# Kernel tuning notes

Hardware: AMD Instinct MI355X
Metric: run time of the kernel (lower is better)

## Reference

```python
import jax, jax.numpy as jnp
import numpy as np

N_NODES = 100000
N_EDGES = 640000
F_IN = 128
HID = 128
N_CLS = 40


def _glorot(key, fan_in, fan_out):
    lim = float(np.sqrt(6.0 / (fan_in + fan_out)))
    return jax.random.uniform(key, (fan_in, fan_out), jnp.float32, -lim, lim)


def setup_inputs() -> dict:
    key = jax.random.key(0)
    ks = jax.random.split(key, 10)
    x = jax.random.normal(ks[0], (N_NODES, F_IN), jnp.float32)
    edge_index = jax.random.randint(ks[1], (2, N_EDGES), 0, N_NODES, jnp.int64 if jax.config.jax_enable_x64 else jnp.int32)
    W1 = _glorot(ks[2], F_IN, HID)
    W2 = _glorot(ks[3], HID, HID)
    W3 = _glorot(ks[4], HID, HID)
    W4 = _glorot(ks[5], HID, N_CLS)
    b1 = jnp.zeros((HID,), jnp.float32)
    b2 = jnp.zeros((HID,), jnp.float32)
    b3 = jnp.zeros((HID,), jnp.float32)
    b4 = jnp.zeros((N_CLS,), jnp.float32)
    return {"x": x, "edge_index": edge_index,
            "W1": W1, "b1": b1, "W2": W2, "b2": b2,
            "W3": W3, "b3": b3, "W4": W4, "b4": b4}


def _prep_edges(edge_index, n):
    # add self-loops, compute symmetric normalization deg^{-1/2}[src]*deg^{-1/2}[dst]
    loop = jnp.arange(n, dtype=edge_index.dtype)
    src = jnp.concatenate([edge_index[0], loop])
    dst = jnp.concatenate([edge_index[1], loop])
    deg = jax.ops.segment_sum(jnp.ones_like(dst, jnp.float32), dst, num_segments=n)
    dinv = jnp.where(deg > 0, jax.lax.rsqrt(deg), 0.0)
    norm = dinv[src] * dinv[dst]  # [E + n]
    return src, dst, norm


def _gcn_conv(x, W, b, src, dst, norm, n):
    h = x @ W                      # dense linear transform [n, out]
    msg = h[src] * norm[:, None]   # gather + scale over edges
    out = jax.ops.segment_sum(msg, dst, num_segments=n)  # scatter-add
    return out + b


def reference(x, edge_index, W1, b1, W2, b2, W3, b3, W4, b4):
    n = x.shape[0]
    src, dst, norm = _prep_edges(edge_index, n)
    h = jax.nn.relu(_gcn_conv(x, W1, b1, src, dst, norm, n))
    h = jax.nn.relu(_gcn_conv(h, W2, b2, src, dst, norm, n))
    h = jax.nn.relu(_gcn_conv(h, W3, b3, src, dst, norm, n))
    h = _gcn_conv(h, W4, b4, src, dst, norm, n)
    return jax.nn.log_softmax(h, axis=1)
```

## Files before the change

### kernel.cpp

```cpp
#include <hip/hip_runtime.h>
#include <math.h>

#define N_NODES 100000
#define N_EDGES 640000

typedef __bf16 bf16x8 __attribute__((ext_vector_type(8)));
typedef float f32x4 __attribute__((ext_vector_type(4)));

__device__ __forceinline__ unsigned short f2b(float x) {
  unsigned int u = __float_as_uint(x);
  u = (u + 0x7FFFu + ((u >> 16) & 1u)) >> 16;
  return (unsigned short)u;
}
__device__ __forceinline__ float blo(unsigned int v) { return __uint_as_float(v << 16); }
__device__ __forceinline__ float bhi(unsigned int v) { return __uint_as_float(v & 0xFFFF0000u); }


__global__ __launch_bounds__(256) void k_count(const int* __restrict__ dst, int* __restrict__ deg, int e) {
  int i = blockIdx.x * 256 + threadIdx.x;
  if (i < e) atomicAdd(&deg[dst[i]], 1);
}

__global__ __launch_bounds__(256) void k_alloc(const int* __restrict__ deg, int* __restrict__ row_ptr,
                                               int* __restrict__ fillpos, int* __restrict__ col,
                                               float* __restrict__ dinv, int* __restrict__ counter, int n) {
  __shared__ int sdata[256];
  __shared__ int sbase;
  int tid = threadIdx.x;
  int i = blockIdx.x * 256 + tid;
  int d = (i < n) ? deg[i] : 0;
  sdata[tid] = d;
  __syncthreads();
  for (int off = 1; off < 256; off <<= 1) {
    int v = (tid >= off) ? sdata[tid - off] : 0;
    __syncthreads();
    sdata[tid] += v;
    __syncthreads();
  }
  if (tid == 255) sbase = atomicAdd(counter, sdata[255]);
  __syncthreads();
  int base = sbase;
  if (i < n) {
    int rp = base + sdata[tid] - d;
    row_ptr[i] = rp;
    fillpos[i] = rp + 1;
    col[rp] = i;
    dinv[i] = rsqrtf((float)d);
  }
}

__global__ __launch_bounds__(256) void k_fill(const int* __restrict__ src, const int* __restrict__ dst,
                                              int* __restrict__ fillpos, int* __restrict__ col, int e) {
  int i = blockIdx.x * 256 + threadIdx.x;
  if (i < e) {
    int d = dst[i];
    int p = atomicAdd(&fillpos[d], 1);
    col[p] = src[i];
  }
}


__global__ __launch_bounds__(256) void k_prep0(const float* __restrict__ W1, const float* __restrict__ W2,
                                               const float* __restrict__ W3, const float* __restrict__ W4,
                                               unsigned short* __restrict__ Wt, unsigned short* __restrict__ Wt4,
                                               unsigned short* __restrict__ Ha, unsigned short* __restrict__ Hc,
                                               unsigned short* __restrict__ H4,
                                               int* __restrict__ deg, int* __restrict__ counter, int n) {
  int b = blockIdx.x;
  int tid = threadIdx.x;
  if (b < 391) {
    int i = b * 256 + tid;
    if (i < n) deg[i] = 1;
    if (i == 0) *counter = 0;
  } else if (b < 583) {
    int bb = b - 391;
    const float* W = (bb < 64) ? W1 : (bb < 128) ? W2 : W3;
    unsigned short* D = Wt + ((bb < 64) ? 0 : (bb < 128) ? 16384 : 32768);
    int idx = (bb & 63) * 256 + tid;
    int k = idx >> 7, nn = idx & 127;
    D[nn * 128 + k] = f2b(W[idx]);
  } else if (b < 607) {
    int idx = (b - 583) * 256 + tid;
    int nn = idx >> 7, k = idx & 127;
    Wt4[nn * 128 + k] = (nn < 40) ? f2b(W4[(size_t)k * 40 + nn]) : (unsigned short)0;
  } else if (b == 607) {
    if (tid < 128) Ha[(size_t)n * 128 + tid] = 0;
    else Hc[(size_t)n * 128 + (tid - 128)] = 0;
  } else {
    if (tid < 48) H4[(size_t)n * 40 + tid] = 0;
  }
}

#define SXP 136


__global__ __launch_bounds__(256) void k_gemm1(const float* __restrict__ X,
                                               const unsigned short* __restrict__ Wt,
                                               const float* __restrict__ dinv,
                                               unsigned short* __restrict__ H, int n) {
  __shared__ unsigned short sW[128 * SXP];
  int tid = threadIdx.x;
  int row0 = blockIdx.x * 64;
  {
    const uint4* Wt4 = (const uint4*)Wt;
#pragma unroll
    for (int i = 0; i < 8; ++i) {
      int f = tid + i * 256;
      *(uint4*)&sW[(f >> 4) * SXP + (f & 15) * 8] = Wt4[f];
    }
  }
  int wave = tid >> 6, lane = tid & 63;
  int m = lane & 15, q = lane >> 4;
  int grow = row0 + wave * 16 + m;
  if (grow >= n) grow = n - 1;
  const float4* X4 = (const float4*)X;
  uint4 a4[4];
#pragma unroll
  for (int kc = 0; kc < 4; ++kc) {
    float4 f0 = X4[(size_t)grow * 32 + kc * 8 + q * 2];
    float4 f1 = X4[(size_t)grow * 32 + kc * 8 + q * 2 + 1];
    a4[kc].x = (unsigned int)f2b(f0.x) | ((unsigned int)f2b(f0.y) << 16);
    a4[kc].y = (unsigned int)f2b(f0.z) | ((unsigned int)f2b(f0.w) << 16);
    a4[kc].z = (unsigned int)f2b(f1.x) | ((unsigned int)f2b(f1.y) << 16);
    a4[kc].w = (unsigned int)f2b(f1.z) | ((unsigned int)f2b(f1.w) << 16);
  }
  __syncthreads();
  f32x4 acc[8];
#pragma unroll
  for (int ct = 0; ct < 8; ++ct) acc[ct] = (f32x4){0.f, 0.f, 0.f, 0.f};
#pragma unroll
  for (int kc = 0; kc < 4; ++kc) {
    bf16x8 a = *(bf16x8*)&a4[kc];
#pragma unroll
    for (int ct = 0; ct < 8; ++ct) {
      bf16x8 b = *(const bf16x8*)&sW[(ct * 16 + m) * SXP + kc * 32 + q * 8];
      acc[ct] = __builtin_amdgcn_mfma_f32_16x16x32_bf16(a, b, acc[ct], 0, 0, 0);
    }
  }
#pragma unroll
  for (int r = 0; r < 4; ++r) {
    int row = row0 + wave * 16 + q * 4 + r;
    if (row < n) {
      float di = dinv[row];
#pragma unroll
      for (int ct = 0; ct < 8; ++ct)
        H[(size_t)row * 128 + ct * 16 + m] = f2b(acc[ct][r] * di);
    }
  }
}


__global__ __launch_bounds__(256) void k_gemmb(const unsigned short* __restrict__ Xb,
                                               const unsigned short* __restrict__ Wt,
                                               const float* __restrict__ dinv,
                                               unsigned short* __restrict__ H, int n) {
  __shared__ unsigned short sW[128 * SXP];
  int tid = threadIdx.x;
  int row0 = blockIdx.x * 64;
  {
    const uint4* Wt4 = (const uint4*)Wt;
#pragma unroll
    for (int i = 0; i < 8; ++i) {
      int f = tid + i * 256;
      *(uint4*)&sW[(f >> 4) * SXP + (f & 15) * 8] = Wt4[f];
    }
  }
  int wave = tid >> 6, lane = tid & 63;
  int m = lane & 15, q = lane >> 4;
  int grow = row0 + wave * 16 + m;
  if (grow >= n) grow = n - 1;
  const uint4* Xb4 = (const uint4*)Xb;
  uint4 a4[4];
#pragma unroll
  for (int kc = 0; kc < 4; ++kc) a4[kc] = Xb4[(size_t)grow * 16 + kc * 4 + q];
  __syncthreads();
  f32x4 acc[8];
#pragma unroll
  for (int ct = 0; ct < 8; ++ct) acc[ct] = (f32x4){0.f, 0.f, 0.f, 0.f};
#pragma unroll
  for (int kc = 0; kc < 4; ++kc) {
    bf16x8 a = *(bf16x8*)&a4[kc];
#pragma unroll
    for (int ct = 0; ct < 8; ++ct) {
      bf16x8 b = *(const bf16x8*)&sW[(ct * 16 + m) * SXP + kc * 32 + q * 8];
      acc[ct] = __builtin_amdgcn_mfma_f32_16x16x32_bf16(a, b, acc[ct], 0, 0, 0);
    }
  }
#pragma unroll
  for (int r = 0; r < 4; ++r) {
    int row = row0 + wave * 16 + q * 4 + r;
    if (row < n) {
      float di = dinv[row];
#pragma unroll
      for (int ct = 0; ct < 8; ++ct)
        H[(size_t)row * 128 + ct * 16 + m] = f2b(acc[ct][r] * di);
    }
  }
}


__global__ __launch_bounds__(256) void k_gemm48(const unsigned short* __restrict__ Xb,
                                                const unsigned short* __restrict__ Wt4,
                                                const float* __restrict__ dinv,
                                                unsigned short* __restrict__ H, int n) {
  __shared__ unsigned short sW[48 * SXP];
  int tid = threadIdx.x;
  int row0 = blockIdx.x * 64;
  {
    const uint4* W4 = (const uint4*)Wt4;
#pragma unroll
    for (int i = 0; i < 3; ++i) {
      int f = tid + i * 256;
      *(uint4*)&sW[(f >> 4) * SXP + (f & 15) * 8] = W4[f];
    }
  }
  int wave = tid >> 6, lane = tid & 63;
  int m = lane & 15, q = lane >> 4;
  int grow = row0 + wave * 16 + m;
  if (grow >= n) grow = n - 1;
  const uint4* Xb4 = (const uint4*)Xb;
  uint4 a4[4];
#pragma unroll
  for (int kc = 0; kc < 4; ++kc) a4[kc] = Xb4[(size_t)grow * 16 + kc * 4 + q];
  __syncthreads();
  f32x4 acc[3];
#pragma unroll
  for (int ct = 0; ct < 3; ++ct) acc[ct] = (f32x4){0.f, 0.f, 0.f, 0.f};
#pragma unroll
  for (int kc = 0; kc < 4; ++kc) {
    bf16x8 a = *(bf16x8*)&a4[kc];
#pragma unroll
    for (int ct = 0; ct < 3; ++ct) {
      bf16x8 b = *(const bf16x8*)&sW[(ct * 16 + m) * SXP + kc * 32 + q * 8];
      acc[ct] = __builtin_amdgcn_mfma_f32_16x16x32_bf16(a, b, acc[ct], 0, 0, 0);
    }
  }
#pragma unroll
  for (int r = 0; r < 4; ++r) {
    int row = row0 + wave * 16 + q * 4 + r;
    if (row < n) {
      float di = dinv[row];
#pragma unroll
      for (int ct = 0; ct < 3; ++ct) {
        int c = ct * 16 + m;
        if (c < 40) H[(size_t)row * 40 + c] = f2b(acc[ct][r] * di);
      }
    }
  }
}


__global__ __launch_bounds__(256) void k_aggb(const unsigned short* __restrict__ H, const int* __restrict__ col,
                                              const int* __restrict__ row_ptr, const int* __restrict__ deg,
                                              const float* __restrict__ dinv, const float* __restrict__ bias,
                                              unsigned short* __restrict__ Xout, int n) {
  int node = blockIdx.x * 16 + (threadIdx.x >> 4);
  int ql = threadIdx.x & 15;
  int qbase = threadIdx.x & 48;
  if (node >= n) return;
  const uint4* H4 = (const uint4*)H;
  int start = row_ptr[node];
  int cnt = deg[node];
  int cnt0 = (cnt < 15) ? cnt : 15;
  int myc = (ql < cnt0) ? col[start + ql] : n;
  float a0 = 0.f, a1 = 0.f, a2 = 0.f, a3 = 0.f, a4 = 0.f, a5 = 0.f, a6 = 0.f, a7 = 0.f;
  for (int base = 0; base < cnt0; base += 8) {
    uint4 v[8];
#pragma unroll
    for (int jj = 0; jj < 8; ++jj) {
      int idx = base + jj;
      idx = (idx > 15) ? 15 : idx;
      int c = __shfl(myc, qbase + idx, 64);
      v[jj] = H4[(size_t)c * 16 + ql];
    }
#pragma unroll
    for (int jj = 0; jj < 8; ++jj) {
      a0 += blo(v[jj].x); a1 += bhi(v[jj].x);
      a2 += blo(v[jj].y); a3 += bhi(v[jj].y);
      a4 += blo(v[jj].z); a5 += bhi(v[jj].z);
      a6 += blo(v[jj].w); a7 += bhi(v[jj].w);
    }
  }
  for (int j = 15; j < cnt; ++j) {
    int c = col[start + j];
    uint4 v = H4[(size_t)c * 16 + ql];
    a0 += blo(v.x); a1 += bhi(v.x);
    a2 += blo(v.y); a3 += bhi(v.y);
    a4 += blo(v.z); a5 += bhi(v.z);
    a6 += blo(v.w); a7 += bhi(v.w);
  }
  float di = dinv[node];
  float4 b0 = ((const float4*)bias)[ql * 2];
  float4 b1 = ((const float4*)bias)[ql * 2 + 1];
  float o0 = fmaf(a0, di, b0.x), o1 = fmaf(a1, di, b0.y);
  float o2 = fmaf(a2, di, b0.z), o3 = fmaf(a3, di, b0.w);
  float o4 = fmaf(a4, di, b1.x), o5 = fmaf(a5, di, b1.y);
  float o6 = fmaf(a6, di, b1.z), o7 = fmaf(a7, di, b1.w);
  o0 = o0 > 0.f ? o0 : 0.f; o1 = o1 > 0.f ? o1 : 0.f;
  o2 = o2 > 0.f ? o2 : 0.f; o3 = o3 > 0.f ? o3 : 0.f;
  o4 = o4 > 0.f ? o4 : 0.f; o5 = o5 > 0.f ? o5 : 0.f;
  o6 = o6 > 0.f ? o6 : 0.f; o7 = o7 > 0.f ? o7 : 0.f;
  uint4 w;
  w.x = (unsigned int)f2b(o0) | ((unsigned int)f2b(o1) << 16);
  w.y = (unsigned int)f2b(o2) | ((unsigned int)f2b(o3) << 16);
  w.z = (unsigned int)f2b(o4) | ((unsigned int)f2b(o5) << 16);
  w.w = (unsigned int)f2b(o6) | ((unsigned int)f2b(o7) << 16);
  ((uint4*)Xout)[(size_t)node * 16 + ql] = w;
}


__global__ __launch_bounds__(256) void k_agg40_lsm(const unsigned short* __restrict__ H, const int* __restrict__ col,
                                                   const int* __restrict__ row_ptr, const int* __restrict__ deg,
                                                   const float* __restrict__ dinv, const float* __restrict__ bias,
                                                   float* __restrict__ out, int n) {
  int node = blockIdx.x * 4 + (threadIdx.x >> 6);
  int lane = threadIdx.x & 63;
  if (node >= n) return;
  const unsigned int* H1 = (const unsigned int*)H;
  int start = row_ptr[node];
  int cnt = deg[node];
  int cnt0 = (cnt < 63) ? cnt : 63;
  int myc = (lane < cnt0) ? col[start + lane] : n;
  int slice = (lane >= 20) + (lane >= 40);
  int pr = lane - slice * 20;
  pr = (pr > 19) ? 19 : pr;
  int rounds = (cnt0 + 2) / 3;
  float ax = 0.f, ay = 0.f;
  for (int rb = 0; rb < rounds; rb += 4) {
    unsigned int v[4];
#pragma unroll
    for (int j = 0; j < 4; ++j) {
      int idx = (rb + j) * 3 + slice;
      idx = (idx > 63) ? 63 : idx;
      int c = __shfl(myc, idx, 64);
      v[j] = H1[(size_t)c * 20 + pr];
    }
#pragma unroll
    for (int j = 0; j < 4; ++j) { ax += blo(v[j]); ay += bhi(v[j]); }
  }
  if (lane < 20) {
    for (int j = 63; j < cnt; ++j) {
      int c = col[start + j];
      unsigned int v = H1[(size_t)c * 20 + pr];
      ax += blo(v);
      ay += bhi(v);
    }
  }
  float ax1 = __shfl(ax, lane + 20, 64), ay1 = __shfl(ay, lane + 20, 64);
  float ax2 = __shfl(ax, lane + 40, 64), ay2 = __shfl(ay, lane + 40, 64);
  float di = dinv[node];
  float2 b2 = ((const float2*)bias)[pr];
  float c0 = fmaf(ax + ax1 + ax2, di, b2.x);
  float c1 = fmaf(ay + ay1 + ay2, di, b2.y);
  float v = (lane < 20) ? fmaxf(c0, c1) : -INFINITY;
#pragma unroll
  for (int off = 32; off > 0; off >>= 1) v = fmaxf(v, __shfl_xor(v, off, 64));
  float e = (lane < 20) ? (__expf(c0 - v) + __expf(c1 - v)) : 0.f;
#pragma unroll
  for (int off = 32; off > 0; off >>= 1) e += __shfl_xor(e, off, 64);
  if (lane < 20) {
    float ls = v + __logf(e);
    ((float2*)out)[(size_t)node * 20 + lane] = make_float2(c0 - ls, c1 - ls);
  }
}


extern "C" void kernel_launch(void* const* d_in, const int* in_sizes, int n_in,
                              void* d_out, int out_size, void* d_ws, size_t ws_size,
                              hipStream_t stream) {
  const float* x  = (const float*)d_in[0];
  const int* edge = (const int*)d_in[1];
  const float* W1 = (const float*)d_in[2];
  const float* b1 = (const float*)d_in[3];
  const float* W2 = (const float*)d_in[4];
  const float* b2 = (const float*)d_in[5];
  const float* W3 = (const float*)d_in[6];
  const float* b3 = (const float*)d_in[7];
  const float* W4 = (const float*)d_in[8];
  const float* b4 = (const float*)d_in[9];
  float* out = (float*)d_out;

  const int n = N_NODES, E = N_EDGES;
  const int* srcp = edge;
  const int* dstp = edge + E;

  char* ws = (char*)d_ws;
  size_t off = 0;
  auto alloc = [&](size_t bytes) -> void* {
    void* p = ws + off;
    off = (off + bytes + 255) & ~(size_t)255;
    return p;
  };
  int*   deg     = (int*)alloc((size_t)n * 4);
  int*   row_ptr = (int*)alloc((size_t)n * 4);
  int*   fillpos = (int*)alloc((size_t)n * 4);
  float* dinv    = (float*)alloc((size_t)n * 4);
  int*   counter = (int*)alloc(256);
  int*   colx    = (int*)alloc((size_t)(E + n) * 4);
  unsigned short* Ha  = (unsigned short*)alloc((size_t)(n + 1) * 128 * 2);
  unsigned short* Hc  = (unsigned short*)alloc((size_t)(n + 1) * 128 * 2);
  unsigned short* Xc  = (unsigned short*)alloc((size_t)n * 128 * 2);
  unsigned short* H4  = (unsigned short*)alloc(((size_t)(n + 1) * 40 + 16) * 2);
  unsigned short* Wt  = (unsigned short*)alloc((size_t)3 * 128 * 128 * 2);
  unsigned short* Wt4 = (unsigned short*)alloc((size_t)48 * 128 * 2);
  (void)ws_size; (void)in_sizes; (void)n_in; (void)out_size;

  k_prep0<<<609, 256, 0, stream>>>(W1, W2, W3, W4, Wt, Wt4, Ha, Hc, H4, deg, counter, n);
  k_count<<<(E + 255) / 256, 256, 0, stream>>>(dstp, deg, E);
  k_alloc<<<(n + 255) / 256, 256, 0, stream>>>(deg, row_ptr, fillpos, colx, dinv, counter, n);
  k_fill <<<(E + 255) / 256, 256, 0, stream>>>(srcp, dstp, fillpos, colx, E);

  const int gg = (n + 63) / 64, ga = (n + 3) / 4, gq = (n + 15) / 16;
  k_gemm1<<<gg, 256, 0, stream>>>(x, Wt, dinv, Ha, n);
  k_aggb <<<gq, 256, 0, stream>>>(Ha, colx, row_ptr, deg, dinv, b1, Xc, n);
  k_gemmb<<<gg, 256, 0, stream>>>(Xc, Wt + 16384, dinv, Hc, n);
  k_aggb <<<gq, 256, 0, stream>>>(Hc, colx, row_ptr, deg, dinv, b2, Xc, n);
  k_gemmb<<<gg, 256, 0, stream>>>(Xc, Wt + 32768, dinv, Ha, n);
  k_aggb <<<gq, 256, 0, stream>>>(Ha, colx, row_ptr, deg, dinv, b3, Xc, n);
  k_gemm48<<<gg, 256, 0, stream>>>(Xc, Wt4, dinv, H4, n);
  k_agg40_lsm<<<ga, 256, 0, stream>>>(H4, colx, row_ptr, deg, dinv, b4, out, n);
}
```

Before: 338.2 us.

## Fuse neighbor aggregation with the following layer's GEMM through shared memory

Merges each aggregation kernel (bias, ReLU, bf16 pack) with the next layer's MFMA GEMM into one templated kernel. The aggregated 64-row tile is staged in LDS and fed straight to the MFMA, which removes the Xc intermediate write and read-back and three kernel launches. The cost is that each 256-thread block now walks 64 nodes in four sequential iterations with a barrier before the GEMM. It also has fewer blocks than the old 16-node aggregation grid, which may reduce latency hiding for the gathers.

```diff
diff --git a/kernel.cpp b/kernel.cpp
--- a/kernel.cpp
+++ b/kernel.cpp
@@ -150,38 +150,111 @@
 }
 
 
-__global__ __launch_bounds__(256) void k_gemmb(const unsigned short* __restrict__ Xb,
-                                               const unsigned short* __restrict__ Wt,
-                                               const float* __restrict__ dinv,
-                                               unsigned short* __restrict__ H, int n) {
-  __shared__ unsigned short sW[128 * SXP];
+template <int NCT>
+__global__ __launch_bounds__(256) void k_fag(const unsigned short* __restrict__ Hin,
+                                             const int* __restrict__ col,
+                                             const int* __restrict__ row_ptr,
+                                             const int* __restrict__ deg,
+                                             const float* __restrict__ dinv,
+                                             const float* __restrict__ bias,
+                                             const unsigned short* __restrict__ Wt,
+                                             unsigned short* __restrict__ Hout, int n) {
+  __shared__ unsigned short sW[NCT * 16 * SXP];
+  __shared__ unsigned short sX[64 * SXP];
   int tid = threadIdx.x;
   int row0 = blockIdx.x * 64;
   {
-    const uint4* Wt4 = (const uint4*)Wt;
-#pragma unroll
-    for (int i = 0; i < 8; ++i) {
+    const uint4* W4 = (const uint4*)Wt;
+#pragma unroll
+    for (int i = 0; i < NCT; ++i) {
       int f = tid + i * 256;
-      *(uint4*)&sW[(f >> 4) * SXP + (f & 15) * 8] = Wt4[f];
-    }
-  }
+      *(uint4*)&sW[(f >> 4) * SXP + (f & 15) * 8] = W4[f];
+    }
+  }
+  int ql = tid & 15;
+  int qbase = tid & 48;
+  const uint4* Hg = (const uint4*)Hin;
+  float4 b0 = ((const float4*)bias)[ql * 2];
+  float4 b1 = ((const float4*)bias)[ql * 2 + 1];
+  int starts[4], cnts[4], mycs[4];
+#pragma unroll
+  for (int it = 0; it < 4; ++it) {
+    int node = row0 + (tid >> 4) + (it << 4);
+    int nc = (node < n) ? node : 0;
+    starts[it] = row_ptr[nc];
+    cnts[it] = deg[nc];
+  }
+#pragma unroll
+  for (int it = 0; it < 4; ++it) {
+    int c0 = (cnts[it] < 15) ? cnts[it] : 15;
+    mycs[it] = (ql < c0) ? col[starts[it] + ql] : n;
+  }
+#pragma unroll 1
+  for (int it = 0; it < 4; ++it) {
+    int node = row0 + (tid >> 4) + (it << 4);
+    if (node >= n) break;
+    int cnt = cnts[it];
+    int cnt0 = (cnt < 15) ? cnt : 15;
+    int myc = mycs[it];
+    float s0 = 0.f, s1 = 0.f, s2 = 0.f, s3 = 0.f, s4 = 0.f, s5 = 0.f, s6 = 0.f, s7 = 0.f;
+    for (int base = 0; base < cnt0; base += 8) {
+      uint4 v[8];
+#pragma unroll
+      for (int jj = 0; jj < 8; ++jj) {
+        int idx = base + jj;
+        idx = (idx > 15) ? 15 : idx;
+        int c = __shfl(myc, qbase + idx, 64);
+        v[jj] = Hg[(size_t)c * 16 + ql];
+      }
+#pragma unroll
+      for (int jj = 0; jj < 8; ++jj) {
+        s0 += blo(v[jj].x); s1 += bhi(v[jj].x);
+        s2 += blo(v[jj].y); s3 += bhi(v[jj].y);
+        s4 += blo(v[jj].z); s5 += bhi(v[jj].z);
+        s6 += blo(v[jj].w); s7 += bhi(v[jj].w);
+      }
+    }
+    for (int j = 15; j < cnt; ++j) {
+      int c = col[starts[it] + j];
+      uint4 v = Hg[(size_t)c * 16 + ql];
+      s0 += blo(v.x); s1 += bhi(v.x);
+      s2 += blo(v.y); s3 += bhi(v.y);
+      s4 += blo(v.z); s5 += bhi(v.z);
+      s6 += blo(v.w); s7 += bhi(v.w);
+    }
+    float di = dinv[node];
+    float o0 = fmaf(s0, di, b0.x), o1 = fmaf(s1, di, b0.y);
+    float o2 = fmaf(s2, di, b0.z), o3 = fmaf(s3, di, b0.w);
+    float o4 = fmaf(s4, di, b1.x), o5 = fmaf(s5, di, b1.y);
+    float o6 = fmaf(s6, di, b1.z), o7 = fmaf(s7, di, b1.w);
+    o0 = o0 > 0.f ? o0 : 0.f; o1 = o1 > 0.f ? o1 : 0.f;
+    o2 = o2 > 0.f ? o2 : 0.f; o3 = o3 > 0.f ? o3 : 0.f;
+    o4 = o4 > 0.f ? o4 : 0.f; o5 = o5 > 0.f ? o5 : 0.f;
+    o6 = o6 > 0.f ? o6 : 0.f; o7 = o7 > 0.f ? o7 : 0.f;
+    uint4 w;
+    w.x = (unsigned int)f2b(o0) | ((unsigned int)f2b(o1) << 16);
+    w.y = (unsigned int)f2b(o2) | ((unsigned int)f2b(o3) << 16);
+    w.z = (unsigned int)f2b(o4) | ((unsigned int)f2b(o5) << 16);
+    w.w = (unsigned int)f2b(o6) | ((unsigned int)f2b(o7) << 16);
+    *(uint4*)&sX[(node - row0) * SXP + ql * 8] = w;
+  }
+  __syncthreads();
   int wave = tid >> 6, lane = tid & 63;
   int m = lane & 15, q = lane >> 4;
   int grow = row0 + wave * 16 + m;
   if (grow >= n) grow = n - 1;
-  const uint4* Xb4 = (const uint4*)Xb;
+  int lrow = grow - row0;
   uint4 a4[4];
 #pragma unroll
-  for (int kc = 0; kc < 4; ++kc) a4[kc] = Xb4[(size_t)grow * 16 + kc * 4 + q];
-  __syncthreads();
-  f32x4 acc[8];
-#pragma unroll
-  for (int ct = 0; ct < 8; ++ct) acc[ct] = (f32x4){0.f, 0.f, 0.f, 0.f};
+  for (int kc = 0; kc < 4; ++kc) a4[kc] = *(const uint4*)&sX[lrow * SXP + kc * 32 + q * 8];
+  f32x4 acc[NCT];
+#pragma unroll
+  for (int ct = 0; ct < NCT; ++ct) acc[ct] = (f32x4){0.f, 0.f, 0.f, 0.f};
 #pragma unroll
   for (int kc = 0; kc < 4; ++kc) {
     bf16x8 a = *(bf16x8*)&a4[kc];
 #pragma unroll
-    for (int ct = 0; ct < 8; ++ct) {
+    for (int ct = 0; ct < NCT; ++ct) {
       bf16x8 b = *(const bf16x8*)&sW[(ct * 16 + m) * SXP + kc * 32 + q * 8];
       acc[ct] = __builtin_amdgcn_mfma_f32_16x16x32_bf16(a, b, acc[ct], 0, 0, 0);
     }
@@ -191,121 +264,19 @@
     int row = row0 + wave * 16 + q * 4 + r;
     if (row < n) {
       float di = dinv[row];
-#pragma unroll
-      for (int ct = 0; ct < 8; ++ct)
-        H[(size_t)row * 128 + ct * 16 + m] = f2b(acc[ct][r] * di);
-    }
-  }
-}
-
-
-__global__ __launch_bounds__(256) void k_gemm48(const unsigned short* __restrict__ Xb,
-                                                const unsigned short* __restrict__ Wt4,
-                                                const float* __restrict__ dinv,
-                                                unsigned short* __restrict__ H, int n) {
-  __shared__ unsigned short sW[48 * SXP];
-  int tid = threadIdx.x;
-  int row0 = blockIdx.x * 64;
-  {
-    const uint4* W4 = (const uint4*)Wt4;
-#pragma unroll
-    for (int i = 0; i < 3; ++i) {
-      int f = tid + i * 256;
-      *(uint4*)&sW[(f >> 4) * SXP + (f & 15) * 8] = W4[f];
-    }
-  }
-  int wave = tid >> 6, lane = tid & 63;
-  int m = lane & 15, q = lane >> 4;
-  int grow = row0 + wave * 16 + m;
-  if (grow >= n) grow = n - 1;
-  const uint4* Xb4 = (const uint4*)Xb;
-  uint4 a4[4];
-#pragma unroll
-  for (int kc = 0; kc < 4; ++kc) a4[kc] = Xb4[(size_t)grow * 16 + kc * 4 + q];
-  __syncthreads();
-  f32x4 acc[3];
-#pragma unroll
-  for (int ct = 0; ct < 3; ++ct) acc[ct] = (f32x4){0.f, 0.f, 0.f, 0.f};
-#pragma unroll
-  for (int kc = 0; kc < 4; ++kc) {
-    bf16x8 a = *(bf16x8*)&a4[kc];
-#pragma unroll
-    for (int ct = 0; ct < 3; ++ct) {
-      bf16x8 b = *(const bf16x8*)&sW[(ct * 16 + m) * SXP + kc * 32 + q * 8];
-      acc[ct] = __builtin_amdgcn_mfma_f32_16x16x32_bf16(a, b, acc[ct], 0, 0, 0);
-    }
-  }
-#pragma unroll
-  for (int r = 0; r < 4; ++r) {
-    int row = row0 + wave * 16 + q * 4 + r;
-    if (row < n) {
-      float di = dinv[row];
-#pragma unroll
-      for (int ct = 0; ct < 3; ++ct) {
-        int c = ct * 16 + m;
-        if (c < 40) H[(size_t)row * 40 + c] = f2b(acc[ct][r] * di);
+      if constexpr (NCT == 8) {
+#pragma unroll
+        for (int ct = 0; ct < 8; ++ct)
+          Hout[(size_t)row * 128 + ct * 16 + m] = f2b(acc[ct][r] * di);
+      } else {
+#pragma unroll
+        for (int ct = 0; ct < NCT; ++ct) {
+          int c = ct * 16 + m;
+          if (c < 40) Hout[(size_t)row * 40 + c] = f2b(acc[ct][r] * di);
+        }
       }
     }
   }
-}
-
-
-__global__ __launch_bounds__(256) void k_aggb(const unsigned short* __restrict__ H, const int* __restrict__ col,
-                                              const int* __restrict__ row_ptr, const int* __restrict__ deg,
-                                              const float* __restrict__ dinv, const float* __restrict__ bias,
-                                              unsigned short* __restrict__ Xout, int n) {
-  int node = blockIdx.x * 16 + (threadIdx.x >> 4);
-  int ql = threadIdx.x & 15;
-  int qbase = threadIdx.x & 48;
-  if (node >= n) return;
-  const uint4* H4 = (const uint4*)H;
-  int start = row_ptr[node];
-  int cnt = deg[node];
-  int cnt0 = (cnt < 15) ? cnt : 15;
-  int myc = (ql < cnt0) ? col[start + ql] : n;
-  float a0 = 0.f, a1 = 0.f, a2 = 0.f, a3 = 0.f, a4 = 0.f, a5 = 0.f, a6 = 0.f, a7 = 0.f;
-  for (int base = 0; base < cnt0; base += 8) {
-    uint4 v[8];
-#pragma unroll
-    for (int jj = 0; jj < 8; ++jj) {
-      int idx = base + jj;
-      idx = (idx > 15) ? 15 : idx;
-      int c = __shfl(myc, qbase + idx, 64);
-      v[jj] = H4[(size_t)c * 16 + ql];
-    }
-#pragma unroll
-    for (int jj = 0; jj < 8; ++jj) {
-      a0 += blo(v[jj].x); a1 += bhi(v[jj].x);
-      a2 += blo(v[jj].y); a3 += bhi(v[jj].y);
-      a4 += blo(v[jj].z); a5 += bhi(v[jj].z);
-      a6 += blo(v[jj].w); a7 += bhi(v[jj].w);
-    }
-  }
-  for (int j = 15; j < cnt; ++j) {
-    int c = col[start + j];
-    uint4 v = H4[(size_t)c * 16 + ql];
-    a0 += blo(v.x); a1 += bhi(v.x);
-    a2 += blo(v.y); a3 += bhi(v.y);
-    a4 += blo(v.z); a5 += bhi(v.z);
-    a6 += blo(v.w); a7 += bhi(v.w);
-  }
-  float di = dinv[node];
-  float4 b0 = ((const float4*)bias)[ql * 2];
-  float4 b1 = ((const float4*)bias)[ql * 2 + 1];
-  float o0 = fmaf(a0, di, b0.x), o1 = fmaf(a1, di, b0.y);
-  float o2 = fmaf(a2, di, b0.z), o3 = fmaf(a3, di, b0.w);
-  float o4 = fmaf(a4, di, b1.x), o5 = fmaf(a5, di, b1.y);
-  float o6 = fmaf(a6, di, b1.z), o7 = fmaf(a7, di, b1.w);
-  o0 = o0 > 0.f ? o0 : 0.f; o1 = o1 > 0.f ? o1 : 0.f;
-  o2 = o2 > 0.f ? o2 : 0.f; o3 = o3 > 0.f ? o3 : 0.f;
-  o4 = o4 > 0.f ? o4 : 0.f; o5 = o5 > 0.f ? o5 : 0.f;
-  o6 = o6 > 0.f ? o6 : 0.f; o7 = o7 > 0.f ? o7 : 0.f;
-  uint4 w;
-  w.x = (unsigned int)f2b(o0) | ((unsigned int)f2b(o1) << 16);
-  w.y = (unsigned int)f2b(o2) | ((unsigned int)f2b(o3) << 16);
-  w.z = (unsigned int)f2b(o4) | ((unsigned int)f2b(o5) << 16);
-  w.w = (unsigned int)f2b(o6) | ((unsigned int)f2b(o7) << 16);
-  ((uint4*)Xout)[(size_t)node * 16 + ql] = w;
 }
 
 
@@ -399,7 +370,6 @@
   int*   colx    = (int*)alloc((size_t)(E + n) * 4);
   unsigned short* Ha  = (unsigned short*)alloc((size_t)(n + 1) * 128 * 2);
   unsigned short* Hc  = (unsigned short*)alloc((size_t)(n + 1) * 128 * 2);
-  unsigned short* Xc  = (unsigned short*)alloc((size_t)n * 128 * 2);
   unsigned short* H4  = (unsigned short*)alloc(((size_t)(n + 1) * 40 + 16) * 2);
   unsigned short* Wt  = (unsigned short*)alloc((size_t)3 * 128 * 128 * 2);
   unsigned short* Wt4 = (unsigned short*)alloc((size_t)48 * 128 * 2);
@@ -410,13 +380,10 @@
   k_alloc<<<(n + 255) / 256, 256, 0, stream>>>(deg, row_ptr, fillpos, colx, dinv, counter, n);
   k_fill <<<(E + 255) / 256, 256, 0, stream>>>(srcp, dstp, fillpos, colx, E);
 
-  const int gg = (n + 63) / 64, ga = (n + 3) / 4, gq = (n + 15) / 16;
+  const int gg = (n + 63) / 64, ga = (n + 3) / 4;
   k_gemm1<<<gg, 256, 0, stream>>>(x, Wt, dinv, Ha, n);
-  k_aggb <<<gq, 256, 0, stream>>>(Ha, colx, row_ptr, deg, dinv, b1, Xc, n);
-  k_gemmb<<<gg, 256, 0, stream>>>(Xc, Wt + 16384, dinv, Hc, n);
-  k_aggb <<<gq, 256, 0, stream>>>(Hc, colx, row_ptr, deg, dinv, b2, Xc, n);
-  k_gemmb<<<gg, 256, 0, stream>>>(Xc, Wt + 32768, dinv, Ha, n);
-  k_aggb <<<gq, 256, 0, stream>>>(Ha, colx, row_ptr, deg, dinv, b3, Xc, n);
-  k_gemm48<<<gg, 256, 0, stream>>>(Xc, Wt4, dinv, H4, n);
+  k_fag<8><<<gg, 256, 0, stream>>>(Ha, colx, row_ptr, deg, dinv, b1, Wt + 16384, Hc, n);
+  k_fag<8><<<gg, 256, 0, stream>>>(Hc, colx, row_ptr, deg, dinv, b2, Wt + 32768, Ha, n);
+  k_fag<3><<<gg, 256, 0, stream>>>(Ha, colx, row_ptr, deg, dinv, b3, Wt4, H4, n);
   k_agg40_lsm<<<ga, 256, 0, stream>>>(H4, colx, row_ptr, deg, dinv, b4, out, n);
 }
```

New measurement: 331.8 us. About the same (-1.9%).
